# Kernel optimization log

Hardware: AMD Instinct MI355X
Metric: run time of the kernel (lower is better)

The kernel has to match this reference:

```python
import jax, jax.numpy as jnp
import numpy as np

DEPTH = 18            # leaf level of complete binary tree (heap layout)
EMB = 128             # encoder.embedding_size
HID = 256             # int(embedding_size * hidden_coef), hidden_coef=2
VAL = 32              # leaf value representation_shape
N_LEAVES = 2 ** DEPTH               # 262144
N_NODES = 2 ** (DEPTH + 1) - 1      # 524287


def setup_inputs() -> dict:
    key = jax.random.key(0)
    ks = jax.random.split(key, 4)
    sc = lambda k, sh, fan: jax.random.normal(k, sh, jnp.float32) * (1.0 / np.sqrt(fan))
    return {
        "leaf_values": jax.random.normal(ks[0], (N_LEAVES, VAL), jnp.float32),
        "We": sc(ks[1], (VAL, EMB), VAL),
        "be": jnp.zeros((EMB,), jnp.float32),
        "W1": sc(ks[2], (2 * EMB, HID), 2 * EMB),
        "b1": jnp.zeros((HID,), jnp.float32),
        "W2": sc(ks[3], (HID, EMB), HID),
        "b2": jnp.zeros((EMB,), jnp.float32),
    }


def reference(leaf_values, We, be, W1, b1, W2, b2):
    lrelu = jax.nn.leaky_relu
    # Embedder: project leaf values into embedding space (simple_dense_embedder)
    leaf_emb = lrelu(leaf_values @ We + be)                  # [N_LEAVES, EMB]
    embs = jnp.zeros((N_NODES, EMB), leaf_emb.dtype)
    leaf_start = 2 ** DEPTH - 1
    embs = embs.at[leaf_start:].set(leaf_emb)                # scatter leaf embeddings
    # Bottom-up: per level, gather children embeddings, run cell MLP, scatter to parents
    for l in range(DEPTH - 1, -1, -1):                       # fixed structural loop (19 levels)
        p0, n = 2 ** l - 1, 2 ** l
        parents = jnp.arange(p0, p0 + n)
        children = jnp.stack([2 * parents + 1, 2 * parents + 2], axis=1).reshape(-1)
        x = embs[children].reshape(n, 2 * EMB)               # gather + reshape [n, arity*EMB]
        h = lrelu(x @ W1 + b1)
        out = lrelu(h @ W2 + b2)                             # [n, EMB]
        embs = embs.at[p0:p0 + n].set(out)                   # scatter_update('embs', ...)
    return embs
```

## Files before the change

### kernel.cpp

```cpp
#include <hip/hip_runtime.h>

#define DEPTH 18
#define EMB 128
#define HID 256
#define VAL 32
#define N_LEAVES (1 << DEPTH)
#define LEAF_START (N_LEAVES - 1)

typedef _Float16 half8 __attribute__((ext_vector_type(8)));
typedef _Float16 half4 __attribute__((ext_vector_type(4)));
typedef float f32x4 __attribute__((ext_vector_type(4)));

__device__ __forceinline__ float lrelu(float x) { return x > 0.f ? x : 0.01f * x; }

__global__ __launch_bounds__(256) void prep_weights(
    const float* __restrict__ W1, const float* __restrict__ W2,
    _Float16* __restrict__ W1f, _Float16* __restrict__ W2f,
    _Float16* __restrict__ W1l, _Float16* __restrict__ W2l)
{
    const int gid = blockIdx.x * 256 + threadIdx.x;
    const int lane = gid & 63;
    const int nn = lane & 15, q = lane >> 4;
    if (gid < 8192) {
        const int f = gid >> 6, kb = f >> 4, jt = f & 15;
        half8 vh, vl;
#pragma unroll
        for (int jj = 0; jj < 8; ++jj) {
            float x = W1[(kb * 32 + q * 8 + jj) * HID + jt * 16 + nn];
            _Float16 h = (_Float16)x;
            vh[jj] = h;
            vl[jj] = (_Float16)(x - (float)h);
        }
        *((half8*)W1f + gid) = vh;
        *((half8*)W1l + gid) = vl;
    } else {
        const int g = gid - 8192;
        const int f = g >> 6, kb = f >> 3, ct = f & 7;
        half8 vh, vl;
#pragma unroll
        for (int jj = 0; jj < 8; ++jj) {
            float x = W2[(kb * 32 + q * 8 + jj) * EMB + ct * 16 + nn];
            _Float16 h = (_Float16)x;
            vh[jj] = h;
            vl[jj] = (_Float16)(x - (float)h);
        }
        *((half8*)W2f + g) = vh;
        *((half8*)W2l + g) = vl;
    }
}

__global__ __launch_bounds__(256) void leaf_embed(
    const float* __restrict__ lv, const float* __restrict__ We,
    const float* __restrict__ be, float* __restrict__ embs)
{
    __shared__ float lvs[16][VAL];
    const int j = threadIdx.x & 127;
    const int h = threadIdx.x >> 7;

    float w[VAL];
#pragma unroll
    for (int k = 0; k < VAL; ++k) w[k] = We[k * EMB + j];
    const float bj = be[j];

    const int leaf0 = blockIdx.x * 16;
    {
        const float* src = lv + (size_t)leaf0 * VAL;
        ((float*)lvs)[threadIdx.x]       = src[threadIdx.x];
        ((float*)lvs)[threadIdx.x + 256] = src[threadIdx.x + 256];
    }
    __syncthreads();

#pragma unroll
    for (int it = 0; it < 8; ++it) {
        const int ll = it * 2 + h;
        float acc = bj;
#pragma unroll
        for (int k4 = 0; k4 < VAL / 4; ++k4) {
            float4 x4 = *(const float4*)&lvs[ll][k4 * 4];
            acc += x4.x * w[k4*4] + x4.y * w[k4*4+1] + x4.z * w[k4*4+2] + x4.w * w[k4*4+3];
        }
        embs[(size_t)(LEAF_START + leaf0 + ll) * EMB + j] = lrelu(acc);
    }
}

__device__ __forceinline__ void strip64(
    const half8 (&w1)[8][2], const half8 (&w2)[8],
    const f32x4 (&bb1)[2], const f32x4 bb2,
    float* __restrict__ embs, int p0, int r0,
    _Float16 (&Xs)[64][264], _Float16 (&Hs)[64][264],
    int tid, int w, int nl, int q)
{
    const float4* src = (const float4*)(embs + ((size_t)(2 * p0 + 1) + 2 * (size_t)r0) * EMB);
#pragma unroll
    for (int i = 0; i < 8; ++i) {
        const int f = i * 512 + tid;
        float4 v = src[f];
        half4 h;
        h[0] = (_Float16)v.x; h[1] = (_Float16)v.y;
        h[2] = (_Float16)v.z; h[3] = (_Float16)v.w;
        *(half4*)&Xs[f >> 6][(f & 63) * 4] = h;
    }
    __syncthreads();

    f32x4 d1[4][2];
#pragma unroll
    for (int s = 0; s < 4; ++s) { d1[s][0] = bb1[0]; d1[s][1] = bb1[1]; }
#pragma unroll
    for (int kb = 0; kb < 8; ++kb) {
#pragma unroll
        for (int s = 0; s < 4; ++s) {
            half8 x = *(const half8*)&Xs[s * 16 + nl][kb * 32 + q * 8];
            d1[s][0] = __builtin_amdgcn_mfma_f32_16x16x32_f16(w1[kb][0], x, d1[s][0], 0, 0, 0);
            d1[s][1] = __builtin_amdgcn_mfma_f32_16x16x32_f16(w1[kb][1], x, d1[s][1], 0, 0, 0);
        }
    }
#pragma unroll
    for (int s = 0; s < 4; ++s) {
#pragma unroll
        for (int j = 0; j < 2; ++j) {
            half4 h;
#pragma unroll
            for (int r = 0; r < 4; ++r) {
                float x = d1[s][j][r];
                h[r] = (_Float16)(x > 0.f ? x : 0.01f * x);
            }
            *(half4*)&Hs[s * 16 + nl][(2 * w + j) * 16 + q * 4] = h;
        }
    }
    __syncthreads();

    f32x4 d2[4];
#pragma unroll
    for (int s = 0; s < 4; ++s) d2[s] = bb2;
#pragma unroll
    for (int kb = 0; kb < 8; ++kb) {
#pragma unroll
        for (int s = 0; s < 4; ++s) {
            half8 h = *(const half8*)&Hs[s * 16 + nl][kb * 32 + q * 8];
            d2[s] = __builtin_amdgcn_mfma_f32_16x16x32_f16(w2[kb], h, d2[s], 0, 0, 0);
        }
    }
    float* obase = embs + ((size_t)p0 + r0) * EMB;
#pragma unroll
    for (int s = 0; s < 4; ++s) {
        f32x4 o;
#pragma unroll
        for (int r = 0; r < 4; ++r) {
            float x = d2[s][r];
            o[r] = x > 0.f ? x : 0.01f * x;
        }
        *(f32x4*)(obase + (s * 16 + nl) * EMB + w * 16 + q * 4) = o;
    }
    __syncthreads();
}

__global__ __launch_bounds__(512) void upper_ladder(
    const _Float16* __restrict__ W1f, const _Float16* __restrict__ W2f,
    const float* __restrict__ b1, const float* __restrict__ b2,
    float* __restrict__ embs)
{
    __shared__ alignas(16) _Float16 Xs[64][264];
    __shared__ alignas(16) _Float16 Hs[64][264];

    const int tid  = threadIdx.x;
    const int w    = tid >> 6;
    const int lane = tid & 63;
    const int nl   = lane & 15;
    const int q    = lane >> 4;
    const int b    = blockIdx.x;

    half8 w1[8][2], w2[8];
#pragma unroll
    for (int kb = 0; kb < 8; ++kb) {
#pragma unroll
        for (int j = 0; j < 2; ++j)
            w1[kb][j] = ((const half8*)W1f)[(kb * 16 + 2 * w + j) * 64 + lane];
        w2[kb] = ((const half8*)W2f)[(kb * 8 + w) * 64 + lane];
    }
    f32x4 bb1[2], bb2;
#pragma unroll
    for (int j = 0; j < 2; ++j)
        bb1[j] = *(const f32x4*)(b1 + (2 * w + j) * 16 + q * 4);
    bb2 = *(const f32x4*)(b2 + w * 16 + q * 4);

#pragma unroll 1
    for (int l = DEPTH - 1; l >= 8; --l) {
        const int p0 = (1 << l) - 1;
        const int R  = 1 << (l - 8);
        const int row0 = R * b;

        if (R >= 64) {
#pragma unroll 1
            for (int t = 0; t < (R >> 6); ++t)
                strip64(w1, w2, bb1, bb2, embs, p0, row0 + t * 64,
                        Xs, Hs, tid, w, nl, q);
        } else {
            const int ns = (R > 16) ? 2 : 1;

            f32x4 d1[2][2];
#pragma unroll
            for (int s = 0; s < 2; ++s) { d1[s][0] = bb1[0]; d1[s][1] = bb1[1]; }
#pragma unroll
            for (int kb = 0; kb < 8; ++kb) {
#pragma unroll
                for (int s = 0; s < 2; ++s) {
                    if (s >= ns) break;
                    const int row = row0 + s * 16 + nl;
                    const float* Xr = embs + (size_t)(2 * (p0 + row) + 1) * EMB
                                    + kb * 32 + q * 8;
                    f32x4 u = *(const f32x4*)Xr;
                    f32x4 v = *(const f32x4*)(Xr + 4);
                    half8 x;
#pragma unroll
                    for (int r = 0; r < 4; ++r) {
                        x[r]     = (_Float16)u[r];
                        x[r + 4] = (_Float16)v[r];
                    }
                    d1[s][0] = __builtin_amdgcn_mfma_f32_16x16x32_f16(w1[kb][0], x, d1[s][0], 0, 0, 0);
                    d1[s][1] = __builtin_amdgcn_mfma_f32_16x16x32_f16(w1[kb][1], x, d1[s][1], 0, 0, 0);
                }
            }
#pragma unroll
            for (int s = 0; s < 2; ++s) {
                if (s >= ns) break;
#pragma unroll
                for (int j = 0; j < 2; ++j) {
                    half4 h;
#pragma unroll
                    for (int r = 0; r < 4; ++r) {
                        float x = d1[s][j][r];
                        h[r] = (_Float16)(x > 0.f ? x : 0.01f * x);
                    }
                    *(half4*)&Hs[s * 16 + nl][(2 * w + j) * 16 + q * 4] = h;
                }
            }
            __syncthreads();

            f32x4 d2[2];
#pragma unroll
            for (int s = 0; s < 2; ++s) d2[s] = bb2;
#pragma unroll
            for (int kb = 0; kb < 8; ++kb) {
#pragma unroll
                for (int s = 0; s < 2; ++s) {
                    if (s >= ns) break;
                    half8 h = *(const half8*)&Hs[s * 16 + nl][kb * 32 + q * 8];
                    d2[s] = __builtin_amdgcn_mfma_f32_16x16x32_f16(w2[kb], h, d2[s], 0, 0, 0);
                }
            }
#pragma unroll
            for (int s = 0; s < 2; ++s) {
                if (s >= ns) break;
                const int idx = s * 16 + nl;
                f32x4 o;
#pragma unroll
                for (int r = 0; r < 4; ++r) {
                    float x = d2[s][r];
                    o[r] = x > 0.f ? x : 0.01f * x;
                }
                if (idx < R)
                    *(f32x4*)(embs + (size_t)(p0 + row0 + idx) * EMB + w * 16 + q * 4) = o;
            }
            __syncthreads();
        }
    }
}

__global__ __launch_bounds__(512) void mid_ladder(
    const _Float16* __restrict__ W1f, const _Float16* __restrict__ W2f,
    const float* __restrict__ b1, const float* __restrict__ b2,
    float* __restrict__ embs)
{
    __shared__ alignas(16) _Float16 Xs[64][264];
    __shared__ alignas(16) _Float16 Hs[64][264];

    const int tid  = threadIdx.x;
    const int w    = tid >> 6;
    const int lane = tid & 63;
    const int nl   = lane & 15;
    const int q    = lane >> 4;

    half8 w1[8][2], w2[8];
#pragma unroll
    for (int kb = 0; kb < 8; ++kb) {
#pragma unroll
        for (int j = 0; j < 2; ++j)
            w1[kb][j] = ((const half8*)W1f)[(kb * 16 + 2 * w + j) * 64 + lane];
        w2[kb] = ((const half8*)W2f)[(kb * 8 + w) * 64 + lane];
    }
    f32x4 bb1[2], bb2;
#pragma unroll
    for (int j = 0; j < 2; ++j)
        bb1[j] = *(const f32x4*)(b1 + (2 * w + j) * 16 + q * 4);
    bb2 = *(const f32x4*)(b2 + w * 16 + q * 4);

    strip64(w1, w2, bb1, bb2, embs, 127,  0, Xs, Hs, tid, w, nl, q);
    strip64(w1, w2, bb1, bb2, embs, 127, 64, Xs, Hs, tid, w, nl, q);
    strip64(w1, w2, bb1, bb2, embs,  63,  0, Xs, Hs, tid, w, nl, q);
}

__global__ __launch_bounds__(512, 2) void tail_levels(
    const _Float16* __restrict__ W1f, const _Float16* __restrict__ W1l,
    const _Float16* __restrict__ W2f, const _Float16* __restrict__ W2l,
    const float* __restrict__ b1, const float* __restrict__ b2,
    float* __restrict__ embs)
{
    __shared__ alignas(16) _Float16 Hsh[32][264];
    __shared__ alignas(16) _Float16 Hsl[32][264];
    __shared__ alignas(16) _Float16 Obh[2][16][136];
    __shared__ alignas(16) _Float16 Obl[2][16][136];

    const int tid  = threadIdx.x;
    const int w    = tid >> 6;
    const int lane = tid & 63;
    const int nl   = lane & 15;
    const int q    = lane >> 4;

    half8 w1h[8][2], w1l[8][2], w2h[8], w2l[8];
#pragma unroll
    for (int kb = 0; kb < 8; ++kb) {
#pragma unroll
        for (int j = 0; j < 2; ++j) {
            const int f = kb * 16 + (2 * w + j);
            w1h[kb][j] = ((const half8*)W1f)[f * 64 + lane];
            w1l[kb][j] = ((const half8*)W1l)[f * 64 + lane];
        }
        const int g = kb * 8 + w;
        w2h[kb] = ((const half8*)W2f)[g * 64 + lane];
        w2l[kb] = ((const half8*)W2l)[g * 64 + lane];
    }

#pragma unroll 1
    for (int l = 5; l >= 0; --l) {
        const int p0 = (1 << l) - 1, n = 1 << l;
        const int ns = (l == 5) ? 2 : 1;

        f32x4 d1[2][2];
#pragma unroll
        for (int s = 0; s < 2; ++s)
#pragma unroll
            for (int j = 0; j < 2; ++j)
                d1[s][j] = *(const f32x4*)(b1 + (2 * w + j) * 16 + q * 4);

#pragma unroll
        for (int kb = 0; kb < 8; ++kb) {
            const int k0  = kb * 32 + q * 8;
            const int hi  = kb >> 2;
            const int col = (kb & 3) * 32 + q * 8;
#pragma unroll
            for (int s = 0; s < 2; ++s) {
                if (s >= ns) break;
                half8 xh, xl;
                if (l == 5) {
                    const int row = s * 16 + nl;
                    const float* Xr = embs + (size_t)(63 + 2 * row) * EMB + k0;
                    f32x4 u = *(const f32x4*)Xr;
                    f32x4 v = *(const f32x4*)(Xr + 4);
#pragma unroll
                    for (int r = 0; r < 4; ++r) {
                        _Float16 a = (_Float16)u[r];
                        xh[r] = a; xl[r] = (_Float16)(u[r] - (float)a);
                        _Float16 b = (_Float16)v[r];
                        xh[r + 4] = b; xl[r + 4] = (_Float16)(v[r] - (float)b);
                    }
                } else {
                    xh = *(const half8*)&Obh[hi][nl][col];
                    xl = *(const half8*)&Obl[hi][nl][col];
                }
#pragma unroll
                for (int j = 0; j < 2; ++j) {
                    d1[s][j] = __builtin_amdgcn_mfma_f32_16x16x32_f16(w1h[kb][j], xh, d1[s][j], 0, 0, 0);
                    d1[s][j] = __builtin_amdgcn_mfma_f32_16x16x32_f16(w1h[kb][j], xl, d1[s][j], 0, 0, 0);
                    d1[s][j] = __builtin_amdgcn_mfma_f32_16x16x32_f16(w1l[kb][j], xh, d1[s][j], 0, 0, 0);
                }
            }
        }

#pragma unroll
        for (int s = 0; s < 2; ++s) {
            if (s >= ns) break;
            const int row = s * 16 + nl;
#pragma unroll
            for (int j = 0; j < 2; ++j) {
                half4 hh4, hl4;
#pragma unroll
                for (int r = 0; r < 4; ++r) {
                    float x = d1[s][j][r];
                    x = x > 0.f ? x : 0.01f * x;
                    _Float16 a = (_Float16)x;
                    hh4[r] = a; hl4[r] = (_Float16)(x - (float)a);
                }
                const int cf = (2 * w + j) * 16 + q * 4;
                *(half4*)&Hsh[row][cf] = hh4;
                *(half4*)&Hsl[row][cf] = hl4;
            }
        }
        __syncthreads();

        f32x4 d2[2];
#pragma unroll
        for (int s = 0; s < 2; ++s)
            d2[s] = *(const f32x4*)(b2 + w * 16 + q * 4);

#pragma unroll
        for (int kb = 0; kb < 8; ++kb) {
#pragma unroll
            for (int s = 0; s < 2; ++s) {
                if (s >= ns) break;
                const int row = s * 16 + nl;
                half8 hh = *(const half8*)&Hsh[row][kb * 32 + q * 8];
                half8 hl = *(const half8*)&Hsl[row][kb * 32 + q * 8];
                d2[s] = __builtin_amdgcn_mfma_f32_16x16x32_f16(w2h[kb], hh, d2[s], 0, 0, 0);
                d2[s] = __builtin_amdgcn_mfma_f32_16x16x32_f16(w2h[kb], hl, d2[s], 0, 0, 0);
                d2[s] = __builtin_amdgcn_mfma_f32_16x16x32_f16(w2l[kb], hh, d2[s], 0, 0, 0);
            }
        }

#pragma unroll
        for (int s = 0; s < 2; ++s) {
            if (s >= ns) break;
            const int row = s * 16 + nl;
            f32x4 o;
#pragma unroll
            for (int r = 0; r < 4; ++r) { float x = d2[s][r]; o[r] = x > 0.f ? x : 0.01f * x; }
            half4 oh4, ol4;
#pragma unroll
            for (int r = 0; r < 4; ++r) {
                _Float16 a = (_Float16)o[r];
                oh4[r] = a; ol4[r] = (_Float16)(o[r] - (float)a);
            }
            const int cf = w * 16 + q * 4;
            *(half4*)&Obh[row & 1][row >> 1][cf] = oh4;
            *(half4*)&Obl[row & 1][row >> 1][cf] = ol4;
            if (row < n)
                *(f32x4*)(embs + (size_t)(p0 + row) * EMB + cf) = o;
        }
        __syncthreads();
    }
}

extern "C" void kernel_launch(void* const* d_in, const int* in_sizes, int n_in,
                              void* d_out, int out_size, void* d_ws, size_t ws_size,
                              hipStream_t stream)
{
    const float* lv = (const float*)d_in[0];
    const float* We = (const float*)d_in[1];
    const float* be = (const float*)d_in[2];
    const float* W1 = (const float*)d_in[3];
    const float* b1 = (const float*)d_in[4];
    const float* W2 = (const float*)d_in[5];
    const float* b2 = (const float*)d_in[6];
    float* embs = (float*)d_out;

    _Float16* W1f = (_Float16*)d_ws;
    _Float16* W2f = W1f + 65536;
    _Float16* W1l = W2f + 32768;
    _Float16* W2l = W1l + 65536;

    prep_weights<<<48, 256, 0, stream>>>(W1, W2, W1f, W2f, W1l, W2l);
    leaf_embed<<<N_LEAVES / 16, 256, 0, stream>>>(lv, We, be, embs);
    upper_ladder<<<256, 512, 0, stream>>>(W1f, W2f, b1, b2, embs);
    mid_ladder<<<1, 512, 0, stream>>>(W1f, W2f, b1, b2, embs);
    tail_levels<<<1, 512, 0, stream>>>(W1f, W1l, W2f, W2l, b1, b2, embs);
}
```

Baseline: 462.9 us.

## Fuse leaf embedding into ladder kernel via split-fp16 MFMA, feeding level 17 from LDS

Drops the separate leaf_embed kernel. Each ladder block now computes its own leaves' embeddings with MFMA, using a hi/lo fp16 split of We and of the leaf values to keep near-fp32 accuracy. It writes the fp32 leaf rows to global memory and also stages their fp16 copies straight into shared memory as input to the level-17 MLP. This removes one kernel launch and the global re-read of leaf embeddings for the first level. In exchange it adds extra MFMA work, more registers for the We fragments, and a longer prep_weights kernel.

```diff
diff --git a/kernel.cpp b/kernel.cpp
--- a/kernel.cpp
+++ b/kernel.cpp
@@ -15,8 +15,10 @@
 
 __global__ __launch_bounds__(256) void prep_weights(
     const float* __restrict__ W1, const float* __restrict__ W2,
+    const float* __restrict__ We,
     _Float16* __restrict__ W1f, _Float16* __restrict__ W2f,
-    _Float16* __restrict__ W1l, _Float16* __restrict__ W2l)
+    _Float16* __restrict__ W1l, _Float16* __restrict__ W2l,
+    _Float16* __restrict__ Wef, _Float16* __restrict__ Wel)
 {
     const int gid = blockIdx.x * 256 + threadIdx.x;
     const int lane = gid & 63;
@@ -33,7 +35,7 @@
         }
         *((half8*)W1f + gid) = vh;
         *((half8*)W1l + gid) = vl;
-    } else {
+    } else if (gid < 12288) {
         const int g = gid - 8192;
         const int f = g >> 6, kb = f >> 3, ct = f & 7;
         half8 vh, vl;
@@ -46,49 +48,86 @@
         }
         *((half8*)W2f + g) = vh;
         *((half8*)W2l + g) = vl;
-    }
-}
-
-__global__ __launch_bounds__(256) void leaf_embed(
-    const float* __restrict__ lv, const float* __restrict__ We,
-    const float* __restrict__ be, float* __restrict__ embs)
-{
-    __shared__ float lvs[16][VAL];
-    const int j = threadIdx.x & 127;
-    const int h = threadIdx.x >> 7;
-
-    float w[VAL];
-#pragma unroll
-    for (int k = 0; k < VAL; ++k) w[k] = We[k * EMB + j];
-    const float bj = be[j];
-
-    const int leaf0 = blockIdx.x * 16;
-    {
-        const float* src = lv + (size_t)leaf0 * VAL;
-        ((float*)lvs)[threadIdx.x]       = src[threadIdx.x];
-        ((float*)lvs)[threadIdx.x + 256] = src[threadIdx.x + 256];
-    }
-    __syncthreads();
-
-#pragma unroll
-    for (int it = 0; it < 8; ++it) {
-        const int ll = it * 2 + h;
-        float acc = bj;
-#pragma unroll
-        for (int k4 = 0; k4 < VAL / 4; ++k4) {
-            float4 x4 = *(const float4*)&lvs[ll][k4 * 4];
-            acc += x4.x * w[k4*4] + x4.y * w[k4*4+1] + x4.z * w[k4*4+2] + x4.w * w[k4*4+3];
-        }
-        embs[(size_t)(LEAF_START + leaf0 + ll) * EMB + j] = lrelu(acc);
-    }
-}
-
-__device__ __forceinline__ void strip64(
+    } else {
+        const int g = gid - 12288;
+        const int ct = g >> 6;
+        half8 vh, vl;
+#pragma unroll
+        for (int jj = 0; jj < 8; ++jj) {
+            float x = We[(q * 8 + jj) * EMB + ct * 16 + nn];
+            _Float16 h = (_Float16)x;
+            vh[jj] = h;
+            vl[jj] = (_Float16)(x - (float)h);
+        }
+        *((half8*)Wef + g) = vh;
+        *((half8*)Wel + g) = vl;
+    }
+}
+
+__device__ __forceinline__ void strip_compute(
     const half8 (&w1)[8][2], const half8 (&w2)[8],
     const f32x4 (&bb1)[2], const f32x4 bb2,
     float* __restrict__ embs, int p0, int r0,
     _Float16 (&Xs)[64][264], _Float16 (&Hs)[64][264],
-    int tid, int w, int nl, int q)
+    int w, int nl, int q)
+{
+    __syncthreads();
+
+    f32x4 d1[4][2];
+#pragma unroll
+    for (int s = 0; s < 4; ++s) { d1[s][0] = bb1[0]; d1[s][1] = bb1[1]; }
+#pragma unroll
+    for (int kb = 0; kb < 8; ++kb) {
+#pragma unroll
+        for (int s = 0; s < 4; ++s) {
+            half8 x = *(const half8*)&Xs[s * 16 + nl][kb * 32 + q * 8];
+            d1[s][0] = __builtin_amdgcn_mfma_f32_16x16x32_f16(w1[kb][0], x, d1[s][0], 0, 0, 0);
+            d1[s][1] = __builtin_amdgcn_mfma_f32_16x16x32_f16(w1[kb][1], x, d1[s][1], 0, 0, 0);
+        }
+    }
+#pragma unroll
+    for (int s = 0; s < 4; ++s) {
+#pragma unroll
+        for (int j = 0; j < 2; ++j) {
+            half4 h;
+#pragma unroll
+            for (int r = 0; r < 4; ++r) {
+                float x = d1[s][j][r];
+                h[r] = (_Float16)(x > 0.f ? x : 0.01f * x);
+            }
+            *(half4*)&Hs[s * 16 + nl][(2 * w + j) * 16 + q * 4] = h;
+        }
+    }
+    __syncthreads();
+
+    f32x4 d2[4];
+#pragma unroll
+    for (int s = 0; s < 4; ++s) d2[s] = bb2;
+#pragma unroll
+    for (int kb = 0; kb < 8; ++kb) {
+#pragma unroll
+        for (int s = 0; s < 4; ++s) {
+            half8 h = *(const half8*)&Hs[s * 16 + nl][kb * 32 + q * 8];
+            d2[s] = __builtin_amdgcn_mfma_f32_16x16x32_f16(w2[kb], h, d2[s], 0, 0, 0);
+        }
+    }
+    float* obase = embs + ((size_t)p0 + r0) * EMB;
+#pragma unroll
+    for (int s = 0; s < 4; ++s) {
+        f32x4 o;
+#pragma unroll
+        for (int r = 0; r < 4; ++r) {
+            float x = d2[s][r];
+            o[r] = x > 0.f ? x : 0.01f * x;
+        }
+        *(f32x4*)(obase + (s * 16 + nl) * EMB + w * 16 + q * 4) = o;
+    }
+    __syncthreads();
+}
+
+__device__ __forceinline__ void stage_global(
+    const float* __restrict__ embs, int p0, int r0,
+    _Float16 (&Xs)[64][264], int tid)
 {
     const float4* src = (const float4*)(embs + ((size_t)(2 * p0 + 1) + 2 * (size_t)r0) * EMB);
 #pragma unroll
@@ -100,62 +139,23 @@
         h[2] = (_Float16)v.z; h[3] = (_Float16)v.w;
         *(half4*)&Xs[f >> 6][(f & 63) * 4] = h;
     }
-    __syncthreads();
-
-    f32x4 d1[4][2];
-#pragma unroll
-    for (int s = 0; s < 4; ++s) { d1[s][0] = bb1[0]; d1[s][1] = bb1[1]; }
-#pragma unroll
-    for (int kb = 0; kb < 8; ++kb) {
-#pragma unroll
-        for (int s = 0; s < 4; ++s) {
-            half8 x = *(const half8*)&Xs[s * 16 + nl][kb * 32 + q * 8];
-            d1[s][0] = __builtin_amdgcn_mfma_f32_16x16x32_f16(w1[kb][0], x, d1[s][0], 0, 0, 0);
-            d1[s][1] = __builtin_amdgcn_mfma_f32_16x16x32_f16(w1[kb][1], x, d1[s][1], 0, 0, 0);
-        }
-    }
-#pragma unroll
-    for (int s = 0; s < 4; ++s) {
-#pragma unroll
-        for (int j = 0; j < 2; ++j) {
-            half4 h;
-#pragma unroll
-            for (int r = 0; r < 4; ++r) {
-                float x = d1[s][j][r];
-                h[r] = (_Float16)(x > 0.f ? x : 0.01f * x);
-            }
-            *(half4*)&Hs[s * 16 + nl][(2 * w + j) * 16 + q * 4] = h;
-        }
-    }
-    __syncthreads();
-
-    f32x4 d2[4];
-#pragma unroll
-    for (int s = 0; s < 4; ++s) d2[s] = bb2;
-#pragma unroll
-    for (int kb = 0; kb < 8; ++kb) {
-#pragma unroll
-        for (int s = 0; s < 4; ++s) {
-            half8 h = *(const half8*)&Hs[s * 16 + nl][kb * 32 + q * 8];
-            d2[s] = __builtin_amdgcn_mfma_f32_16x16x32_f16(w2[kb], h, d2[s], 0, 0, 0);
-        }
-    }
-    float* obase = embs + ((size_t)p0 + r0) * EMB;
-#pragma unroll
-    for (int s = 0; s < 4; ++s) {
-        f32x4 o;
-#pragma unroll
-        for (int r = 0; r < 4; ++r) {
-            float x = d2[s][r];
-            o[r] = x > 0.f ? x : 0.01f * x;
-        }
-        *(f32x4*)(obase + (s * 16 + nl) * EMB + w * 16 + q * 4) = o;
-    }
-    __syncthreads();
-}
-
-__global__ __launch_bounds__(512) void upper_ladder(
+}
+
+__device__ __forceinline__ void strip64(
+    const half8 (&w1)[8][2], const half8 (&w2)[8],
+    const f32x4 (&bb1)[2], const f32x4 bb2,
+    float* __restrict__ embs, int p0, int r0,
+    _Float16 (&Xs)[64][264], _Float16 (&Hs)[64][264],
+    int tid, int w, int nl, int q)
+{
+    stage_global(embs, p0, r0, Xs, tid);
+    strip_compute(w1, w2, bb1, bb2, embs, p0, r0, Xs, Hs, w, nl, q);
+}
+
+__global__ __launch_bounds__(512) void tree_ladder(
     const _Float16* __restrict__ W1f, const _Float16* __restrict__ W2f,
+    const _Float16* __restrict__ Wef, const _Float16* __restrict__ Wel,
+    const float* __restrict__ lv, const float* __restrict__ be,
     const float* __restrict__ b1, const float* __restrict__ b2,
     float* __restrict__ embs)
 {
@@ -177,14 +177,55 @@
             w1[kb][j] = ((const half8*)W1f)[(kb * 16 + 2 * w + j) * 64 + lane];
         w2[kb] = ((const half8*)W2f)[(kb * 8 + w) * 64 + lane];
     }
-    f32x4 bb1[2], bb2;
+    const half8 wef = ((const half8*)Wef)[w * 64 + lane];
+    const half8 wel = ((const half8*)Wel)[w * 64 + lane];
+    f32x4 bb1[2], bb2, bbe;
 #pragma unroll
     for (int j = 0; j < 2; ++j)
         bb1[j] = *(const f32x4*)(b1 + (2 * w + j) * 16 + q * 4);
     bb2 = *(const f32x4*)(b2 + w * 16 + q * 4);
-
+    bbe = *(const f32x4*)(be + w * 16 + q * 4);
+
+    {
+        const int p0 = (1 << 17) - 1;
 #pragma unroll 1
-    for (int l = DEPTH - 1; l >= 8; --l) {
+        for (int t = 0; t < 8; ++t) {
+            const int r0 = 512 * b + t * 64;
+#pragma unroll
+            for (int tile = 0; tile < 8; ++tile) {
+                const int ll = tile * 16 + nl;
+                const float* lvr = lv + ((size_t)2 * r0 + ll) * VAL + q * 8;
+                f32x4 u = *(const f32x4*)lvr;
+                f32x4 v = *(const f32x4*)(lvr + 4);
+                half8 xh, xl;
+#pragma unroll
+                for (int r = 0; r < 4; ++r) {
+                    _Float16 a = (_Float16)u[r];
+                    xh[r] = a; xl[r] = (_Float16)(u[r] - (float)a);
+                    _Float16 g = (_Float16)v[r];
+                    xh[r + 4] = g; xl[r + 4] = (_Float16)(v[r] - (float)g);
+                }
+                f32x4 e = bbe;
+                e = __builtin_amdgcn_mfma_f32_16x16x32_f16(wef, xh, e, 0, 0, 0);
+                e = __builtin_amdgcn_mfma_f32_16x16x32_f16(wef, xl, e, 0, 0, 0);
+                e = __builtin_amdgcn_mfma_f32_16x16x32_f16(wel, xh, e, 0, 0, 0);
+                f32x4 o;
+                half4 h4;
+#pragma unroll
+                for (int r = 0; r < 4; ++r) {
+                    float x = e[r];
+                    o[r] = x > 0.f ? x : 0.01f * x;
+                    h4[r] = (_Float16)o[r];
+                }
+                *(f32x4*)(embs + (size_t)(LEAF_START + 2 * r0 + ll) * EMB + w * 16 + q * 4) = o;
+                *(half4*)&Xs[ll >> 1][(ll & 1) * 128 + w * 16 + q * 4] = h4;
+            }
+            strip_compute(w1, w2, bb1, bb2, embs, p0, r0, Xs, Hs, w, nl, q);
+        }
+    }
+
+#pragma unroll 1
+    for (int l = 16; l >= 8; --l) {
         const int p0 = (1 << l) - 1;
         const int R  = 1 << (l - 8);
         const int row0 = R * b;
@@ -456,10 +497,11 @@
     _Float16* W2f = W1f + 65536;
     _Float16* W1l = W2f + 32768;
     _Float16* W2l = W1l + 65536;
-
-    prep_weights<<<48, 256, 0, stream>>>(W1, W2, W1f, W2f, W1l, W2l);
-    leaf_embed<<<N_LEAVES / 16, 256, 0, stream>>>(lv, We, be, embs);
-    upper_ladder<<<256, 512, 0, stream>>>(W1f, W2f, b1, b2, embs);
+    _Float16* Wef = W2l + 32768;
+    _Float16* Wel = Wef + 4096;
+
+    prep_weights<<<50, 256, 0, stream>>>(W1, W2, We, W1f, W2f, W1l, W2l, Wef, Wel);
+    tree_ladder<<<256, 512, 0, stream>>>(W1f, W2f, Wef, Wel, lv, be, b1, b2, embs);
     mid_ladder<<<1, 512, 0, stream>>>(W1f, W2f, b1, b2, embs);
     tail_levels<<<1, 512, 0, stream>>>(W1f, W1l, W2f, W2l, b1, b2, embs);
 }
```

Result: no change. 455.4 us (-1.6%).
